# Kernel tuning notes

Hardware: AMD Instinct MI355X
Metric: run time of the kernel (lower is better)

## Reference

```python
import jax, jax.numpy as jnp
import numpy as np

D = 256
H = 4
HD = D // H


def setup_inputs() -> dict:
    key = jax.random.key(0)
    ks = jax.random.split(key, 12)
    A, T = 64, 512
    s = 1.0 / np.sqrt(D)
    return {
        "features": jax.random.normal(ks[0], (A, T, D), jnp.float32),
        "positions": jax.random.normal(ks[1], (A, T, 2), jnp.float32),
        "Wq": jax.random.normal(ks[2], (D, D), jnp.float32) * s,
        "bq": jnp.zeros((D,), jnp.float32),
        "Wk": jax.random.normal(ks[3], (D, D), jnp.float32) * s,
        "bk": jnp.zeros((D,), jnp.float32),
        "Wv": jax.random.normal(ks[4], (D, D), jnp.float32) * s,
        "bv": jnp.zeros((D,), jnp.float32),
        "Wo": jax.random.normal(ks[5], (D, D), jnp.float32) * s,
        "bo": jnp.zeros((D,), jnp.float32),
        "max_distance": 2,
        "time_window": 64,
    }


def _sparse_mask(positions, max_distance, time_window):
    # positions: [A, T, 2] -> allowed [A, T, T]
    A, T, _ = positions.shape
    diff = positions[:, :, None, :] - positions[:, None, :, :]  # [A,T,T,2]
    dist2 = jnp.sum(diff * diff, axis=-1)                       # [A,T,T]
    t = jnp.arange(T)
    tmask = jnp.abs(t[:, None] - t[None, :]) <= time_window      # [T,T]
    return (dist2 <= float(max_distance) ** 2) & tmask[None]     # [A,T,T]


def reference(features, positions, Wq, bq, Wk, bk, Wv, bv, Wo, bo,
              max_distance, time_window):
    A, T, Dm = features.shape
    allowed = _sparse_mask(positions, max_distance, time_window)  # [A,T,T]
    q = features @ Wq.T + bq
    k = features @ Wk.T + bk
    v = features @ Wv.T + bv
    # split heads: [A, T, H, HD]
    q = q.reshape(A, T, H, HD)
    k = k.reshape(A, T, H, HD)
    v = v.reshape(A, T, H, HD)
    scale = 1.0 / np.sqrt(HD)
    scores = jnp.einsum("athd,ashd->ahts", q, k) * scale          # [A,H,T,T]
    scores = jnp.where(allowed[:, None], scores, -jnp.inf)
    attn = jax.nn.softmax(scores, axis=-1)
    out = jnp.einsum("ahts,ashd->athd", attn, v).reshape(A, T, Dm)
    return out @ Wo.T + bo
```

## Files before the change

kernel.cpp:

```cpp
#include <hip/hip_runtime.h>
#include <hip/hip_bf16.h>
#include <cstdint>
#include <cstddef>

typedef __attribute__((ext_vector_type(8))) _Float16 half8;
typedef __attribute__((ext_vector_type(4))) _Float16 half4v;
typedef __attribute__((ext_vector_type(4))) float floatx4;

#define MFMA16(a, b, c) __builtin_amdgcn_mfma_f32_16x16x32_f16((a), (b), (c), 0, 0, 0)

#define GLOAD_LDS16(g, l)                                                     \
    __builtin_amdgcn_global_load_lds(                                         \
        (const __attribute__((address_space(1))) void*)(g),                   \
        (__attribute__((address_space(3))) void*)(l), 16, 0, 0)

#define NFEAT 8388608
#define NW    65536
#define NCVT  8448

__global__ __launch_bounds__(256) void convert_kernel(
    const float* __restrict__ feat, const float* __restrict__ wq,
    const float* __restrict__ wk, const float* __restrict__ wv,
    const float* __restrict__ wo, const float* __restrict__ positions,
    const int* __restrict__ mdp, const int* __restrict__ twp,
    _Float16* __restrict__ out, uint64_t* __restrict__ maskbuf)
{
    if (blockIdx.x >= NCVT) {
        const int n2 = blockIdx.x - NCVT;
        const int a = n2 >> 3, qt = n2 & 7;
        const int q0 = qt * 64, s_base = q0 - 64;
        const int tid = threadIdx.x, lane = tid & 63, wid = tid >> 6;
        const int quad = lane >> 4, l16 = lane & 15;
        const size_t abase = (size_t)a * 512;
        const int md = *mdp, tw = *twp;
        const float md2 = (float)(md * md);

        float qpx[4], qpy[4];
        int trow[4];
#pragma unroll
        for (int r = 0; r < 4; ++r) {
            int m = wid * 16 + quad * 4 + r;
            trow[r] = q0 + m;
            float2 qp = *(const float2*)(positions + (abase + q0 + m) * 2);
            qpx[r] = qp.x;
            qpy[r] = qp.y;
        }
        uint64_t ok_bits = 0;
#pragma unroll
        for (int j = 0; j < 12; ++j) {
            int si = j * 16 + l16;
            int sr = s_base + si;
            int sc = min(max(sr, 0), 511);
            float2 kp = *(const float2*)(positions + (abase + sc) * 2);
            bool svalid = (sr >= 0) && (sr < 512);
#pragma unroll
            for (int r = 0; r < 4; ++r) {
                float dx = qpx[r] - kp.x, dy = qpy[r] - kp.y;
                float d2 = dx * dx + dy * dy;
                int dt = trow[r] - sr; dt = dt < 0 ? -dt : dt;
                if (svalid && (d2 <= md2) && (dt <= tw))
                    ok_bits |= (1ull << (j * 4 + r));
            }
        }
        maskbuf[(size_t)n2 * 256 + tid] = ok_bits;
        return;
    }

    long tid  = (long)blockIdx.x * blockDim.x + threadIdx.x;
    long base = tid * 4;
    const float* src;
    long off;
    if (base < NFEAT) { src = feat; off = base; }
    else {
        long r = base - NFEAT;
        int  w = (int)(r >> 16);
        off = r & (NW - 1);
        src = (w == 0) ? wq : (w == 1) ? wk : (w == 2) ? wv : wo;
    }
    float4 v = *(const float4*)(src + off);
    half4v h = { (_Float16)v.x, (_Float16)v.y, (_Float16)v.z, (_Float16)v.w };
    *(half4v*)(out + base) = h;
}

__global__ __launch_bounds__(256) void qkv_fused(
    const _Float16* __restrict__ featH, const _Float16* __restrict__ WH,
    const float* __restrict__ bq, const float* __restrict__ bk,
    const float* __restrict__ bv,
    _Float16* __restrict__ Qb, _Float16* __restrict__ Kb, _Float16* __restrict__ Vb)
{
    __shared__ _Float16 Xs[4 * 128 * 64];
    __shared__ _Float16 Ws[128 * 64];

    const int n   = blockIdx.x;
    const int idx = n >> 3;
    const int bm  = (n & 7) * 32 + (idx >> 1);
    const int bn  = idx & 1;

    const int tid  = threadIdx.x;
    const int lane = tid & 63, wid = tid >> 6;
    const int quad = lane >> 4, l16 = lane & 15;
    const int wm = wid & 1, wn = wid >> 1;

    int wrow[4], wchd[4];
#pragma unroll
    for (int i = 0; i < 4; ++i) {
        int g = tid + 256 * i;
        wrow[i] = g >> 3;
        wchd[i] = g & 7;
    }
    half8 pw[4];
    auto loadW = [&](int t) {
        const _Float16* base = WH + (size_t)(t >> 2) * NW
                             + (size_t)bn * 32768 + (t & 3) * 64;
#pragma unroll
        for (int i = 0; i < 4; ++i) {
            int chs = wchd[i] ^ (wrow[i] & 7);
            pw[i] = *(const half8*)(base + (size_t)wrow[i] * 256 + chs * 8);
        }
    };
    auto storeW = [&]() {
#pragma unroll
        for (int i = 0; i < 4; ++i)
            *(half8*)(&Ws[wrow[i] * 64 + wchd[i] * 8]) = pw[i];
    };

    loadW(0);

    const _Float16* Xg = featH + (size_t)bm * 128 * 256;
#pragma unroll
    for (int sl = 0; sl < 4; ++sl)
#pragma unroll
        for (int i = 0; i < 4; ++i) {
            int grp = wid * 4 + i;
            int row = grp * 8 + (lane >> 3);
            int sc  = (lane & 7) ^ (row & 7);
            GLOAD_LDS16(Xg + (size_t)row * 256 + sl * 64 + sc * 8,
                        Xs + sl * 8192 + grp * 512);
        }

    const float* bz[3] = { bq, bk, bv };
    _Float16*    oz[3] = { Qb, Kb, Vb };

    storeW();
    floatx4 acc[4][4] = {};

#pragma unroll 1
    for (int t = 0; t < 12; ++t) {
        __syncthreads();
        if (t < 11) loadW(t + 1);
        const int ks = t & 3;
#pragma unroll
        for (int kh = 0; kh < 2; ++kh) {
            half8 af[4], bf[4];
#pragma unroll
            for (int mi = 0; mi < 4; ++mi) {
                int row = wm * 64 + mi * 16 + l16;
                int cs  = (kh * 4 + quad) ^ (row & 7);
                af[mi] = *(const half8*)(&Xs[ks * 8192 + row * 64 + cs * 8]);
            }
#pragma unroll
            for (int ni = 0; ni < 4; ++ni) {
                int row = wn * 64 + ni * 16 + l16;
                int cs  = (kh * 4 + quad) ^ (row & 7);
                bf[ni] = *(const half8*)(&Ws[row * 64 + cs * 8]);
            }
#pragma unroll
            for (int mi = 0; mi < 4; ++mi)
#pragma unroll
                for (int ni = 0; ni < 4; ++ni)
                    acc[mi][ni] = MFMA16(af[mi], bf[ni], acc[mi][ni]);
        }
        __syncthreads();
        if (t < 11) storeW();
        if ((t & 3) == 3) {
            const int z = t >> 2;
            const float* bias = bz[z];
            _Float16*    outp = oz[z];
#pragma unroll
            for (int ni = 0; ni < 4; ++ni) {
                int col = bn * 128 + wn * 64 + ni * 16 + l16;
                float bv2 = bias[col];
#pragma unroll
                for (int mi = 0; mi < 4; ++mi) {
#pragma unroll
                    for (int r = 0; r < 4; ++r) {
                        int row = bm * 128 + wm * 64 + mi * 16 + quad * 4 + r;
                        outp[(size_t)row * 256 + col] =
                            (_Float16)(acc[mi][ni][r] + bv2);
                    }
                    acc[mi][ni] = floatx4{0.f, 0.f, 0.f, 0.f};
                }
            }
        }
    }
}

__global__ __launch_bounds__(256) void attn_kernel(
    const _Float16* __restrict__ Qb, const _Float16* __restrict__ Kb,
    const _Float16* __restrict__ Vb, const uint64_t* __restrict__ maskbuf,
    _Float16* __restrict__ attnb)
{
    const int n   = blockIdx.x;
    const int idx = n >> 3;
    const int a   = (n & 7) * 8 + (idx >> 5);
    const int rem = idx & 31;
    const int qt  = rem >> 2, h = rem & 3;

    const int q0 = qt * 64;
    const int s_base = q0 - 64;
    const int tid = threadIdx.x, lane = tid & 63, wid = tid >> 6;
    const int quad = lane >> 4, l16 = lane & 15;

    __shared__ _Float16 KPs[192 * 64];
    __shared__ _Float16 Vt[64 * 192];

    const size_t abase = (size_t)a * 512;

    const uint64_t ok_bits = maskbuf[(size_t)(a * 8 + qt) * 256 + tid];

    const size_t qrow = abase + q0 + wid * 16 + l16;
    half8 aq0 = *(const half8*)(Qb + qrow * 256 + h * 64 + quad * 8);
    half8 aq1 = *(const half8*)(Qb + qrow * 256 + h * 64 + 32 + quad * 8);

#pragma unroll
    for (int i = 0; i < 6; ++i) {
        int grp = wid * 6 + i;
        int si  = grp * 8 + (lane >> 3);
        int sc  = min(max(s_base + si, 0), 511);
        int ch  = (lane & 7) ^ (si & 7);
        GLOAD_LDS16(Kb + (abase + sc) * 256 + h * 64 + ch * 8, KPs + grp * 512);
    }
#pragma unroll
    for (int i = 0; i < 3; ++i) {
        int g   = tid + 256 * i;
        int si2 = (g % 96) * 2;
        int d0  = (g / 96) * 8;
        int sa  = min(max(s_base + si2, 0), 511);
        int sb  = min(max(s_base + si2 + 1, 0), 511);
        half8 v0 = *(const half8*)(Vb + (abase + sa) * 256 + h * 64 + d0);
        half8 v1 = *(const half8*)(Vb + (abase + sb) * 256 + h * 64 + d0);
        int c = si2 >> 3;
#pragma unroll
        for (int j = 0; j < 8; ++j) {
            int d  = d0 + j;
            int cs = (c & ~7) | ((c & 7) ^ (d & 7));
            union { _Float16 hh[2]; uint32_t u; } p;
            p.hh[0] = v0[j]; p.hh[1] = v1[j];
            *(uint32_t*)(&Vt[d * 192 + cs * 8 + (si2 & 7)]) = p.u;
        }
    }
    __syncthreads();

    floatx4 S[12];
#pragma unroll
    for (int j = 0; j < 12; ++j) {
        int si = j * 16 + l16;
        half8 bk0 = *(const half8*)(&KPs[si * 64 + ((quad) ^ (si & 7)) * 8]);
        half8 bk1 = *(const half8*)(&KPs[si * 64 + ((4 + quad) ^ (si & 7)) * 8]);
        floatx4 acc = {};
        acc = MFMA16(aq0, bk0, acc);
        acc = MFMA16(aq1, bk1, acc);
#pragma unroll
        for (int r = 0; r < 4; ++r) {
            bool ok = (ok_bits >> (j * 4 + r)) & 1;
            S[j][r] = __expf(ok ? acc[r] * 0.125f : -1e30f);
        }
    }

    float minv[4];
#pragma unroll
    for (int r = 0; r < 4; ++r) {
        float l = 0.f;
#pragma unroll
        for (int j = 0; j < 12; ++j) l += S[j][r];
        l += __shfl_xor(l, 1);
        l += __shfl_xor(l, 2);
        l += __shfl_xor(l, 4);
        l += __shfl_xor(l, 8);
        minv[r] = 1.0f / l;
    }

    __syncthreads();

    _Float16* Ps = KPs + wid * (16 * 192);
#pragma unroll
    for (int j = 0; j < 12; ++j)
#pragma unroll
        for (int r = 0; r < 4; ++r) {
            int row = quad * 4 + r;
            int col = j * 16 + l16;
            int ch  = (col >> 3) ^ (row & 7);
            Ps[row * 192 + ch * 8 + (col & 7)] = (_Float16)(S[j][r] * minv[r]);
        }

    half8 af[6];
#pragma unroll
    for (int k = 0; k < 6; ++k) {
        int ch = (k * 4 + quad) ^ (l16 & 7);
        af[k] = *(const half8*)(&Ps[l16 * 192 + ch * 8]);
    }
#pragma unroll
    for (int nn = 0; nn < 4; ++nn) {
        floatx4 accO = {};
#pragma unroll
        for (int k = 0; k < 6; ++k) {
            int row = nn * 16 + l16;
            int c   = k * 4 + quad;
            int cs  = (c & ~7) | ((c & 7) ^ (row & 7));
            half8 bv = *(const half8*)(&Vt[row * 192 + cs * 8]);
            accO = MFMA16(af[k], bv, accO);
        }
#pragma unroll
        for (int r = 0; r < 4; ++r) {
            int row = q0 + wid * 16 + quad * 4 + r;
            attnb[(abase + row) * 256 + h * 64 + nn * 16 + l16] = (_Float16)accO[r];
        }
    }
}

__global__ __launch_bounds__(256) void out_gemm(
    const _Float16* __restrict__ attnH, const _Float16* __restrict__ WoH,
    const float* __restrict__ bo, float* __restrict__ out)
{
    __shared__ _Float16 Xs[4 * 128 * 64];
    __shared__ _Float16 Ws[128 * 64];

    const int n   = blockIdx.x;
    const int idx = n >> 3;
    const int bm  = (n & 7) * 32 + (idx >> 1);
    const int bn  = idx & 1;

    const int tid  = threadIdx.x;
    const int lane = tid & 63, wid = tid >> 6;
    const int quad = lane >> 4, l16 = lane & 15;
    const int wm = wid & 1, wn = wid >> 1;

    int wrow[4], wchd[4];
#pragma unroll
    for (int i = 0; i < 4; ++i) {
        int g = tid + 256 * i;
        wrow[i] = g >> 3;
        wchd[i] = g & 7;
    }
    half8 pw[4];
    auto loadW = [&](int t) {
        const _Float16* base = WoH + (size_t)bn * 32768 + t * 64;
#pragma unroll
        for (int i = 0; i < 4; ++i) {
            int chs = wchd[i] ^ (wrow[i] & 7);
            pw[i] = *(const half8*)(base + (size_t)wrow[i] * 256 + chs * 8);
        }
    };
    auto storeW = [&]() {
#pragma unroll
        for (int i = 0; i < 4; ++i)
            *(half8*)(&Ws[wrow[i] * 64 + wchd[i] * 8]) = pw[i];
    };

    loadW(0);

    const _Float16* Ag = attnH + (size_t)bm * 128 * 256;
#pragma unroll
    for (int sl = 0; sl < 4; ++sl)
#pragma unroll
        for (int i = 0; i < 4; ++i) {
            int grp = wid * 4 + i;
            int row = grp * 8 + (lane >> 3);
            int sc  = (lane & 7) ^ (row & 7);
            GLOAD_LDS16(Ag + (size_t)row * 256 + sl * 64 + sc * 8,
                        Xs + sl * 8192 + grp * 512);
        }

    storeW();
    floatx4 acc[4][4] = {};

#pragma unroll 1
    for (int t = 0; t < 4; ++t) {
        __syncthreads();
        if (t < 3) loadW(t + 1);
#pragma unroll
        for (int kh = 0; kh < 2; ++kh) {
            half8 af[4], bf[4];
#pragma unroll
            for (int mi = 0; mi < 4; ++mi) {
                int row = wm * 64 + mi * 16 + l16;
                int cs  = (kh * 4 + quad) ^ (row & 7);
                af[mi] = *(const half8*)(&Xs[t * 8192 + row * 64 + cs * 8]);
            }
#pragma unroll
            for (int ni = 0; ni < 4; ++ni) {
                int row = wn * 64 + ni * 16 + l16;
                int cs  = (kh * 4 + quad) ^ (row & 7);
                bf[ni] = *(const half8*)(&Ws[row * 64 + cs * 8]);
            }
#pragma unroll
            for (int mi = 0; mi < 4; ++mi)
#pragma unroll
                for (int ni = 0; ni < 4; ++ni)
                    acc[mi][ni] = MFMA16(af[mi], bf[ni], acc[mi][ni]);
        }
        __syncthreads();
        if (t < 3) storeW();
    }

#pragma unroll
    for (int ni = 0; ni < 4; ++ni) {
        int col = bn * 128 + wn * 64 + ni * 16 + l16;
        float bv = bo[col];
#pragma unroll
        for (int mi = 0; mi < 4; ++mi)
#pragma unroll
            for (int r = 0; r < 4; ++r) {
                int row = bm * 128 + wm * 64 + mi * 16 + quad * 4 + r;
                out[(size_t)row * 256 + col] = acc[mi][ni][r] + bv;
            }
    }
}

extern "C" void kernel_launch(void* const* d_in, const int* in_sizes, int n_in,
                              void* d_out, int out_size, void* d_ws, size_t ws_size,
                              hipStream_t stream)
{
    const float* feat = (const float*)d_in[0];
    const float* pos  = (const float*)d_in[1];
    const float* Wq   = (const float*)d_in[2];
    const float* bq   = (const float*)d_in[3];
    const float* Wk   = (const float*)d_in[4];
    const float* bk   = (const float*)d_in[5];
    const float* Wv   = (const float*)d_in[6];
    const float* bv   = (const float*)d_in[7];
    const float* Wo   = (const float*)d_in[8];
    const float* bo   = (const float*)d_in[9];
    const int*   md   = (const int*)d_in[10];
    const int*   tw   = (const int*)d_in[11];
    float*       out  = (float*)d_out;

    _Float16* ws    = (_Float16*)d_ws;
    _Float16* featH = ws;
    _Float16* WH    = featH + NFEAT;
    _Float16* WoHp  = WH + 3 * (size_t)NW;
    _Float16* Qb    = WH + 4 * (size_t)NW;
    _Float16* Kb    = Qb + NFEAT;
    _Float16* Vb    = Kb + NFEAT;
    _Float16* attnH = Vb + NFEAT;
    uint64_t* maskb = (uint64_t*)(attnH + NFEAT);

    convert_kernel<<<NCVT + 512, 256, 0, stream>>>(
        feat, Wq, Wk, Wv, Wo, pos, md, tw, ws, maskb);

    qkv_fused<<<512, 256, 0, stream>>>(featH, WH, bq, bk, bv, Qb, Kb, Vb);

    attn_kernel<<<2048, 256, 0, stream>>>(Qb, Kb, Vb, maskb, attnH);

    out_gemm<<<512, 256, 0, stream>>>(attnH, WoHp, bo, out);
}
```

Before: 169.2 us.

## Load weights and K directly from global memory, drop LDS staging

The QKV and output GEMMs stop staging weight tiles through shared memory. Each wave now reads its B fragments straight from global memory (cache-resident weights), which removes the per-step barriers and the LDS store pipeline. The attention kernel likewise reads K fragments directly from global memory instead of an LDS tile. The P matrix goes through a small per-wave buffer, written in chunks interleaved with the PV MFMAs. This cuts LDS footprint and synchronisation, which may raise occupancy, but exposes more global-load latency and uncoalesced fragment reads.

```diff
diff --git a/kernel.cpp b/kernel.cpp
--- a/kernel.cpp
+++ b/kernel.cpp
@@ -89,7 +89,6 @@
     _Float16* __restrict__ Qb, _Float16* __restrict__ Kb, _Float16* __restrict__ Vb)
 {
     __shared__ _Float16 Xs[4 * 128 * 64];
-    __shared__ _Float16 Ws[128 * 64];
 
     const int n   = blockIdx.x;
     const int idx = n >> 3;
@@ -100,31 +99,6 @@
     const int lane = tid & 63, wid = tid >> 6;
     const int quad = lane >> 4, l16 = lane & 15;
     const int wm = wid & 1, wn = wid >> 1;
-
-    int wrow[4], wchd[4];
-#pragma unroll
-    for (int i = 0; i < 4; ++i) {
-        int g = tid + 256 * i;
-        wrow[i] = g >> 3;
-        wchd[i] = g & 7;
-    }
-    half8 pw[4];
-    auto loadW = [&](int t) {
-        const _Float16* base = WH + (size_t)(t >> 2) * NW
-                             + (size_t)bn * 32768 + (t & 3) * 64;
-#pragma unroll
-        for (int i = 0; i < 4; ++i) {
-            int chs = wchd[i] ^ (wrow[i] & 7);
-            pw[i] = *(const half8*)(base + (size_t)wrow[i] * 256 + chs * 8);
-        }
-    };
-    auto storeW = [&]() {
-#pragma unroll
-        for (int i = 0; i < 4; ++i)
-            *(half8*)(&Ws[wrow[i] * 64 + wchd[i] * 8]) = pw[i];
-    };
-
-    loadW(0);
 
     const _Float16* Xg = featH + (size_t)bm * 128 * 256;
 #pragma unroll
@@ -137,60 +111,52 @@
             GLOAD_LDS16(Xg + (size_t)row * 256 + sl * 64 + sc * 8,
                         Xs + sl * 8192 + grp * 512);
         }
+    __syncthreads();
 
     const float* bz[3] = { bq, bk, bv };
     _Float16*    oz[3] = { Qb, Kb, Vb };
 
-    storeW();
-    floatx4 acc[4][4] = {};
-
 #pragma unroll 1
-    for (int t = 0; t < 12; ++t) {
-        __syncthreads();
-        if (t < 11) loadW(t + 1);
-        const int ks = t & 3;
-#pragma unroll
-        for (int kh = 0; kh < 2; ++kh) {
-            half8 af[4], bf[4];
-#pragma unroll
-            for (int mi = 0; mi < 4; ++mi) {
-                int row = wm * 64 + mi * 16 + l16;
-                int cs  = (kh * 4 + quad) ^ (row & 7);
-                af[mi] = *(const half8*)(&Xs[ks * 8192 + row * 64 + cs * 8]);
+    for (int z = 0; z < 3; ++z) {
+        const _Float16* Wb = WH + (size_t)z * NW + (size_t)bn * 32768
+                           + (size_t)(wn * 64 + l16) * 256 + quad * 8;
+        floatx4 acc[4][4] = {};
+#pragma unroll
+        for (int ks = 0; ks < 4; ++ks)
+#pragma unroll
+            for (int kh = 0; kh < 2; ++kh) {
+                half8 af[4], bf[4];
+#pragma unroll
+                for (int ni = 0; ni < 4; ++ni)
+                    bf[ni] = *(const half8*)(Wb + (size_t)ni * 16 * 256
+                                             + ks * 64 + kh * 32);
+#pragma unroll
+                for (int mi = 0; mi < 4; ++mi) {
+                    int row = wm * 64 + mi * 16 + l16;
+                    int cs  = (kh * 4 + quad) ^ (row & 7);
+                    af[mi] = *(const half8*)(&Xs[ks * 8192 + row * 64 + cs * 8]);
+                }
+#pragma unroll
+                for (int mi = 0; mi < 4; ++mi)
+#pragma unroll
+                    for (int ni = 0; ni < 4; ++ni)
+                        acc[mi][ni] = MFMA16(af[mi], bf[ni], acc[mi][ni]);
             }
-#pragma unroll
-            for (int ni = 0; ni < 4; ++ni) {
-                int row = wn * 64 + ni * 16 + l16;
-                int cs  = (kh * 4 + quad) ^ (row & 7);
-                bf[ni] = *(const half8*)(&Ws[row * 64 + cs * 8]);
-            }
+
+        const float* bias = bz[z];
+        _Float16*    outp = oz[z];
+#pragma unroll
+        for (int ni = 0; ni < 4; ++ni) {
+            int col = bn * 128 + wn * 64 + ni * 16 + l16;
+            float bv2 = bias[col];
 #pragma unroll
             for (int mi = 0; mi < 4; ++mi)
 #pragma unroll
-                for (int ni = 0; ni < 4; ++ni)
-                    acc[mi][ni] = MFMA16(af[mi], bf[ni], acc[mi][ni]);
-        }
-        __syncthreads();
-        if (t < 11) storeW();
-        if ((t & 3) == 3) {
-            const int z = t >> 2;
-            const float* bias = bz[z];
-            _Float16*    outp = oz[z];
-#pragma unroll
-            for (int ni = 0; ni < 4; ++ni) {
-                int col = bn * 128 + wn * 64 + ni * 16 + l16;
-                float bv2 = bias[col];
-#pragma unroll
-                for (int mi = 0; mi < 4; ++mi) {
-#pragma unroll
-                    for (int r = 0; r < 4; ++r) {
-                        int row = bm * 128 + wm * 64 + mi * 16 + quad * 4 + r;
-                        outp[(size_t)row * 256 + col] =
-                            (_Float16)(acc[mi][ni][r] + bv2);
-                    }
-                    acc[mi][ni] = floatx4{0.f, 0.f, 0.f, 0.f};
+                for (int r = 0; r < 4; ++r) {
+                    int row = bm * 128 + wm * 64 + mi * 16 + quad * 4 + r;
+                    outp[(size_t)row * 256 + col] =
+                        (_Float16)(acc[mi][ni][r] + bv2);
                 }
-            }
         }
     }
 }
@@ -211,25 +177,16 @@
     const int tid = threadIdx.x, lane = tid & 63, wid = tid >> 6;
     const int quad = lane >> 4, l16 = lane & 15;
 
-    __shared__ _Float16 KPs[192 * 64];
     __shared__ _Float16 Vt[64 * 192];
+    __shared__ _Float16 Pbuf[4 * 16 * 40];
 
     const size_t abase = (size_t)a * 512;
-
     const uint64_t ok_bits = maskbuf[(size_t)(a * 8 + qt) * 256 + tid];
 
     const size_t qrow = abase + q0 + wid * 16 + l16;
     half8 aq0 = *(const half8*)(Qb + qrow * 256 + h * 64 + quad * 8);
     half8 aq1 = *(const half8*)(Qb + qrow * 256 + h * 64 + 32 + quad * 8);
 
-#pragma unroll
-    for (int i = 0; i < 6; ++i) {
-        int grp = wid * 6 + i;
-        int si  = grp * 8 + (lane >> 3);
-        int sc  = min(max(s_base + si, 0), 511);
-        int ch  = (lane & 7) ^ (si & 7);
-        GLOAD_LDS16(Kb + (abase + sc) * 256 + h * 64 + ch * 8, KPs + grp * 512);
-    }
 #pragma unroll
     for (int i = 0; i < 3; ++i) {
         int g   = tid + 256 * i;
@@ -255,8 +212,10 @@
 #pragma unroll
     for (int j = 0; j < 12; ++j) {
         int si = j * 16 + l16;
-        half8 bk0 = *(const half8*)(&KPs[si * 64 + ((quad) ^ (si & 7)) * 8]);
-        half8 bk1 = *(const half8*)(&KPs[si * 64 + ((4 + quad) ^ (si & 7)) * 8]);
+        int sc = min(max(s_base + si, 0), 511);
+        const _Float16* kp = Kb + (abase + sc) * 256 + h * 64 + quad * 8;
+        half8 bk0 = *(const half8*)(kp);
+        half8 bk1 = *(const half8*)(kp + 32);
         floatx4 acc = {};
         acc = MFMA16(aq0, bk0, acc);
         acc = MFMA16(aq1, bk1, acc);
@@ -280,42 +239,37 @@
         minv[r] = 1.0f / l;
     }
 
-    __syncthreads();
-
-    _Float16* Ps = KPs + wid * (16 * 192);
-#pragma unroll
-    for (int j = 0; j < 12; ++j)
-#pragma unroll
-        for (int r = 0; r < 4; ++r) {
-            int row = quad * 4 + r;
-            int col = j * 16 + l16;
-            int ch  = (col >> 3) ^ (row & 7);
-            Ps[row * 192 + ch * 8 + (col & 7)] = (_Float16)(S[j][r] * minv[r]);
-        }
-
-    half8 af[6];
+    _Float16* P = Pbuf + wid * (16 * 40);
+    floatx4 accO[4] = {};
 #pragma unroll
     for (int k = 0; k < 6; ++k) {
-        int ch = (k * 4 + quad) ^ (l16 & 7);
-        af[k] = *(const half8*)(&Ps[l16 * 192 + ch * 8]);
-    }
-#pragma unroll
-    for (int nn = 0; nn < 4; ++nn) {
-        floatx4 accO = {};
-#pragma unroll
-        for (int k = 0; k < 6; ++k) {
+#pragma unroll
+        for (int jj = 0; jj < 2; ++jj) {
+            int j = 2 * k + jj;
+#pragma unroll
+            for (int r = 0; r < 4; ++r)
+                P[(quad * 4 + r) * 40 + jj * 16 + l16] =
+                    (_Float16)(S[j][r] * minv[r]);
+        }
+        half8 af = *(const half8*)(&P[l16 * 40 + quad * 8]);
+#pragma unroll
+        for (int nn = 0; nn < 4; ++nn) {
             int row = nn * 16 + l16;
             int c   = k * 4 + quad;
             int cs  = (c & ~7) | ((c & 7) ^ (row & 7));
             half8 bv = *(const half8*)(&Vt[row * 192 + cs * 8]);
-            accO = MFMA16(af[k], bv, accO);
-        }
+            accO[nn] = MFMA16(af, bv, accO[nn]);
+        }
+    }
+
+#pragma unroll
+    for (int nn = 0; nn < 4; ++nn)
 #pragma unroll
         for (int r = 0; r < 4; ++r) {
             int row = q0 + wid * 16 + quad * 4 + r;
-            attnb[(abase + row) * 256 + h * 64 + nn * 16 + l16] = (_Float16)accO[r];
-        }
-    }
+            attnb[(abase + row) * 256 + h * 64 + nn * 16 + l16] =
+                (_Float16)accO[nn][r];
+        }
 }
 
 __global__ __launch_bounds__(256) void out_gemm(
@@ -323,7 +277,6 @@
     const float* __restrict__ bo, float* __restrict__ out)
 {
     __shared__ _Float16 Xs[4 * 128 * 64];
-    __shared__ _Float16 Ws[128 * 64];
 
     const int n   = blockIdx.x;
     const int idx = n >> 3;
@@ -334,30 +287,6 @@
     const int lane = tid & 63, wid = tid >> 6;
     const int quad = lane >> 4, l16 = lane & 15;
     const int wm = wid & 1, wn = wid >> 1;
-
-    int wrow[4], wchd[4];
-#pragma unroll
-    for (int i = 0; i < 4; ++i) {
-        int g = tid + 256 * i;
-        wrow[i] = g >> 3;
-        wchd[i] = g & 7;
-    }
-    half8 pw[4];
-    auto loadW = [&](int t) {
-        const _Float16* base = WoH + (size_t)bn * 32768 + t * 64;
-#pragma unroll
-        for (int i = 0; i < 4; ++i) {
-            int chs = wchd[i] ^ (wrow[i] & 7);
-            pw[i] = *(const half8*)(base + (size_t)wrow[i] * 256 + chs * 8);
-        }
-    };
-    auto storeW = [&]() {
-#pragma unroll
-        for (int i = 0; i < 4; ++i)
-            *(half8*)(&Ws[wrow[i] * 64 + wchd[i] * 8]) = pw[i];
-    };
-
-    loadW(0);
 
     const _Float16* Ag = attnH + (size_t)bm * 128 * 256;
 #pragma unroll
@@ -370,28 +299,25 @@
             GLOAD_LDS16(Ag + (size_t)row * 256 + sl * 64 + sc * 8,
                         Xs + sl * 8192 + grp * 512);
         }
-
-    storeW();
+    __syncthreads();
+
+    const _Float16* Wb = WoH + (size_t)bn * 32768
+                       + (size_t)(wn * 64 + l16) * 256 + quad * 8;
     floatx4 acc[4][4] = {};
-
-#pragma unroll 1
-    for (int t = 0; t < 4; ++t) {
-        __syncthreads();
-        if (t < 3) loadW(t + 1);
+#pragma unroll
+    for (int ks = 0; ks < 4; ++ks)
 #pragma unroll
         for (int kh = 0; kh < 2; ++kh) {
             half8 af[4], bf[4];
+#pragma unroll
+            for (int ni = 0; ni < 4; ++ni)
+                bf[ni] = *(const half8*)(Wb + (size_t)ni * 16 * 256
+                                         + ks * 64 + kh * 32);
 #pragma unroll
             for (int mi = 0; mi < 4; ++mi) {
                 int row = wm * 64 + mi * 16 + l16;
                 int cs  = (kh * 4 + quad) ^ (row & 7);
-                af[mi] = *(const half8*)(&Xs[t * 8192 + row * 64 + cs * 8]);
-            }
-#pragma unroll
-            for (int ni = 0; ni < 4; ++ni) {
-                int row = wn * 64 + ni * 16 + l16;
-                int cs  = (kh * 4 + quad) ^ (row & 7);
-                bf[ni] = *(const half8*)(&Ws[row * 64 + cs * 8]);
+                af[mi] = *(const half8*)(&Xs[ks * 8192 + row * 64 + cs * 8]);
             }
 #pragma unroll
             for (int mi = 0; mi < 4; ++mi)
@@ -399,9 +325,6 @@
                 for (int ni = 0; ni < 4; ++ni)
                     acc[mi][ni] = MFMA16(af[mi], bf[ni], acc[mi][ni]);
         }
-        __syncthreads();
-        if (t < 3) storeW();
-    }
 
 #pragma unroll
     for (int ni = 0; ni < 4; ++ni) {
```

New measurement: 201.3 us. 1.19x slower.
